# Optimization experiments

Measured on AMD Instinct MI355X. Metric: run time of the kernel, lower is better.

Reference implementation:

```python
import jax, jax.numpy as jnp
import numpy as np

D = 768      # d_model (BERT-base)
H = 8        # MatTransformer heads
DK = D // H  # 96
L = 4        # MatTransformer layers
FF = 1024    # MatTransformer hidden_size
NREL = 97    # num_relations
BAG = 8      # bag_len (docs per bag)
SEQ = 512    # seq_len
NB = 3       # bridge entities per doc
S = 2 + NB   # spans per doc: h, t, bridges
E = BAG * S  # total entities = 40
NEG = -1e30


def setup_inputs() -> dict:
    key = jax.random.key(0)
    ks = jax.random.split(key, 30)
    w = lambda k, shp: jax.random.normal(k, shp, jnp.float32) * 0.02
    inp = {
        "embedding": jax.random.normal(ks[0], (BAG, SEQ, D), jnp.float32),
        "spans": jnp.sort(jax.random.randint(ks[1], (BAG, S, 2), 0, SEQ, jnp.int32), axis=-1),
        # Codred pairwise-relation params (torch Linear stored as [in, out])
        "wu_w": w(ks[2], (D, D)), "wu_b": jnp.zeros((D,), jnp.float32),
        "wvv_w": w(ks[3], (D, D)), "wvv_b": jnp.zeros((D,), jnp.float32),
        "lnr_w": w(ks[4], (D, D)), "lnr_b": jnp.zeros((D,), jnp.float32),
        # MatTransformer params, stacked over layers
        "matt_wq": w(ks[5], (L, D, D)), "matt_bq": jnp.zeros((L, D), jnp.float32),
        "matt_wk": w(ks[6], (L, D, D)), "matt_bk": jnp.zeros((L, D), jnp.float32),
        "matt_wv": w(ks[7], (L, D, D)), "matt_bv": jnp.zeros((L, D), jnp.float32),
        "matt_wo": w(ks[8], (L, D, D)), "matt_bo": jnp.zeros((L, D), jnp.float32),
        "matt_w1": w(ks[9], (L, D, FF)), "matt_b1": jnp.zeros((L, FF), jnp.float32),
        "matt_w2": w(ks[10], (L, FF, D)), "matt_b2": jnp.zeros((L, D), jnp.float32),
        "matt_g1": jnp.ones((L, D), jnp.float32), "matt_be1": jnp.zeros((L, D), jnp.float32),
        "matt_g2": jnp.ones((L, D), jnp.float32), "matt_be2": jnp.zeros((L, D), jnp.float32),
        # relation predictor
        "pred_w": w(ks[11], (D, NREL)), "pred_b": jnp.zeros((NREL,), jnp.float32),
    }
    return inp


def _layernorm(x, g, b, eps=1e-5):
    m = jnp.mean(x, axis=-1, keepdims=True)
    v = jnp.var(x, axis=-1, keepdims=True)
    return (x - m) * jax.lax.rsqrt(v + eps) * g + b


def reference(embedding, spans, wu_w, wu_b, wvv_w, wvv_b, lnr_w, lnr_b,
              matt_wq, matt_bq, matt_wk, matt_bk, matt_wv, matt_bv, matt_wo, matt_bo,
              matt_w1, matt_b1, matt_w2, matt_b2, matt_g1, matt_be1, matt_g2, matt_be2,
              pred_w, pred_b):
    # --- entity span max-pool (gather + max over inclusive [start, end]) ---
    pos = jnp.arange(SEQ)
    span_mask = (pos[None, None, :] >= spans[..., 0:1]) & (pos[None, None, :] <= spans[..., 1:2])  # [BAG,S,SEQ]
    pooled = jnp.max(jnp.where(span_mask[..., None], embedding[:, None, :, :], NEG), axis=2)  # [BAG,S,D]
    htb = pooled.reshape(E, D)  # per-doc order: h, t, b1..bNB (matches htb_embs stacking)

    # --- pairwise relation matrix: relu(ln1(relu(u_i + v_j))) ---
    u = htb @ wu_w + wu_b                       # [E,D]
    v = htb @ wvv_w + wvv_b                     # [E,D]
    alpha = jax.nn.relu(u[:, None, :] + v[None, :, :])          # [E,E,D]
    rel = jax.nn.relu(alpha @ lnr_w + lnr_b)                    # [E,E,D]

    # --- MatTransformer: encoder over the E*E relation tokens (rel_mask all ones) ---
    T = E * E
    x = rel.reshape(T, D)
    scale = 1.0 / np.sqrt(DK).astype(np.float32)
    for l in range(L):
        q = (x @ matt_wq[l] + matt_bq[l]).reshape(T, H, DK)
        k = (x @ matt_wk[l] + matt_bk[l]).reshape(T, H, DK)
        vv = (x @ matt_wv[l] + matt_bv[l]).reshape(T, H, DK)
        scores = jnp.einsum('thd,shd->hts', q, k) * scale       # [H,T,T]
        attn = jax.nn.softmax(scores, axis=-1)
        o = jnp.einsum('hts,shd->thd', attn, vv).reshape(T, D)
        o = o @ matt_wo[l] + matt_bo[l]
        x = _layernorm(x + o, matt_g1[l], matt_be1[l])
        ff = jax.nn.relu(x @ matt_w1[l] + matt_b1[l]) @ matt_w2[l] + matt_b2[l]
        x = _layernorm(x + ff, matt_g2[l], matt_be2[l])
    rel_m = x.reshape(E, E, D)

    # --- gather (h, t) relation features, predict, bag max-pool over logits ---
    h_pos = jnp.arange(BAG) * S      # head entity index per doc
    t_pos = h_pos + 1                # tail entity index per doc
    ht_feat = rel_m[h_pos, t_pos]    # [BAG,D]
    ht_logits = ht_feat @ pred_w + pred_b          # [BAG,NREL]
    bag_logit = jnp.max(ht_logits, axis=0, keepdims=True)  # [1,NREL]
    return bag_logit
```

## Files before the change

kernel.cpp:

```cpp
#include <hip/hip_runtime.h>


#define D    768
#define H    8
#define DKD  96
#define LAY  4
#define FFD  1024
#define NREL 97
#define BAG  8
#define SPANS 5
#define E    40
#define TT   1600
#define SEQ  512
#define D3   2304
#define NS   3

typedef __attribute__((ext_vector_type(8))) short bf16x8;
typedef __attribute__((ext_vector_type(4))) float f32x4;
typedef unsigned short ushort_t;
typedef unsigned int uint_t;

__device__ __forceinline__ ushort_t f2b(float x) {
    uint_t u = __builtin_bit_cast(uint_t, x);
    return (ushort_t)((u + 0x7fffu + ((u >> 16) & 1u)) >> 16);
}
__device__ __forceinline__ float b2f(ushort_t v) {
    return __builtin_bit_cast(float, (uint_t)v << 16);
}

__device__ __forceinline__ void gload16(const void* g, void* l) {
    __builtin_amdgcn_global_load_lds(
        (const __attribute__((address_space(1))) unsigned int*)g,
        (__attribute__((address_space(3))) unsigned int*)l, 16, 0, 0);
}

__device__ __forceinline__ float block_sum(float v, float* red) {
#pragma unroll
    for (int o = 32; o >= 1; o >>= 1) v += __shfl_xor(v, o);
    __syncthreads();
    if ((threadIdx.x & 63) == 0) red[threadIdx.x >> 6] = v;
    __syncthreads();
    return red[0] + red[1] + red[2] + red[3];
}

__global__ __launch_bounds__(256) void span_pool_p1(const float* __restrict__ emb,
        const int* __restrict__ spans, float* __restrict__ partial) {
    const int e = blockIdx.x, pg = blockIdx.y;
    const int bag = e / SPANS;
    const int st = spans[e * 2 + 0];
    const int en = spans[e * 2 + 1];
    const int p0 = max(st, pg * 64);
    const int p1 = min(en, pg * 64 + 63);
    const int tid = threadIdx.x;
    if (tid >= 192) return;
    float4 m = make_float4(-1e30f, -1e30f, -1e30f, -1e30f);
    for (int p = p0; p <= p1; ++p) {
        const float4 v = *(const float4*)(emb + ((size_t)bag * SEQ + p) * D + tid * 4);
        m.x = fmaxf(m.x, v.x); m.y = fmaxf(m.y, v.y);
        m.z = fmaxf(m.z, v.z); m.w = fmaxf(m.w, v.w);
    }
    *(float4*)(partial + ((size_t)e * 8 + pg) * D + tid * 4) = m;
}

__global__ __launch_bounds__(256) void span_pool_p2(const float* __restrict__ partial,
        ushort_t* __restrict__ htb) {
    const int e = blockIdx.x;
    const int tid = threadIdx.x;
    if (tid >= 192) return;
    float4 m = make_float4(-1e30f, -1e30f, -1e30f, -1e30f);
#pragma unroll
    for (int pg = 0; pg < 8; ++pg) {
        const float4 v = *(const float4*)(partial + ((size_t)e * 8 + pg) * D + tid * 4);
        m.x = fmaxf(m.x, v.x); m.y = fmaxf(m.y, v.y);
        m.z = fmaxf(m.z, v.z); m.w = fmaxf(m.w, v.w);
    }
    ushort4 o;
    o.x = f2b(m.x); o.y = f2b(m.y); o.z = f2b(m.z); o.w = f2b(m.w);
    *(ushort4*)(htb + (size_t)e * D + tid * 4) = o;
}

__global__ __launch_bounds__(256) void alpha_k(const float* __restrict__ uv,
        ushort_t* __restrict__ a) {
    const int ij = blockIdx.x;
    const int i = ij / E, j = ij % E;
    const int tid = threadIdx.x;
#pragma unroll
    for (int t2 = 0; t2 < 3; ++t2) {
        const int d = tid + t2 * 256;
        a[(size_t)ij * D + d] =
            f2b(fmaxf(uv[(size_t)i * 1536 + d] + uv[(size_t)j * 1536 + 768 + d], 0.f));
    }
}

__global__ __launch_bounds__(256) void transpose_up(const float* __restrict__ lnr,
        const float* __restrict__ wu, const float* __restrict__ wvv,
        ushort_t* __restrict__ lnrT, ushort_t* __restrict__ wuvT) {
    __shared__ float t[32][33];
    const int z = blockIdx.z;
    const float* src = (z == 0) ? lnr : (z == 1) ? wu : wvv;
    ushort_t* dst = (z == 0) ? lnrT : wuvT + (size_t)(z - 1) * D * D;
    const int n0 = blockIdx.x * 32, k0 = blockIdx.y * 32;
    const int tx = threadIdx.x & 31, ty = threadIdx.x >> 5;
#pragma unroll
    for (int i = 0; i < 4; ++i)
        t[ty + i * 8][tx] = src[(size_t)(k0 + ty + i * 8) * D + n0 + tx];
    __syncthreads();
#pragma unroll
    for (int i = 0; i < 4; ++i)
        dst[(size_t)(n0 + ty + i * 8) * D + k0 + tx] = f2b(t[tx][ty + i * 8]);
}

__global__ __launch_bounds__(256) void transpose_layer(const float* __restrict__ wq,
        const float* __restrict__ wk, const float* __restrict__ wv,
        const float* __restrict__ wo, const float* __restrict__ w1,
        const float* __restrict__ w2, int l, ushort_t* __restrict__ wT4,
        ushort_t* __restrict__ w1T, ushort_t* __restrict__ w2T) {
    __shared__ float t[32][33];
    const int z = blockIdx.z;
    const float* src; ushort_t* dst; int K, N;
    if (z < 4) {
        K = D; N = D;
        src = (z == 0 ? wq : z == 1 ? wk : z == 2 ? wv : wo) + (size_t)l * D * D;
        dst = wT4 + (size_t)z * D * D;
    } else if (z == 4) {
        K = D; N = FFD; src = w1 + (size_t)l * D * FFD; dst = w1T;
    } else {
        K = FFD; N = D; src = w2 + (size_t)l * FFD * D; dst = w2T;
    }
    const int n0 = blockIdx.x * 32, k0 = blockIdx.y * 32;
    if (n0 >= N || k0 >= K) return;
    const int tx = threadIdx.x & 31, ty = threadIdx.x >> 5;
#pragma unroll
    for (int i = 0; i < 4; ++i)
        t[ty + i * 8][tx] = src[(size_t)(k0 + ty + i * 8) * N + n0 + tx];
    __syncthreads();
#pragma unroll
    for (int i = 0; i < 4; ++i)
        dst[(size_t)(n0 + ty + i * 8) * K + k0 + tx] = f2b(t[tx][ty + i * 8]);
}

__global__ __launch_bounds__(256) void concat_bias(const float* __restrict__ bq,
        const float* __restrict__ bk, const float* __restrict__ bv,
        const float* __restrict__ bu, const float* __restrict__ bvv,
        float* __restrict__ bqkv, float* __restrict__ buv) {
    const int i = blockIdx.x * 256 + threadIdx.x;
    if (i < LAY * D3) {
        const int l = i / D3, j = i % D3;
        bqkv[i] = j < D ? bq[l * D + j] : j < 2 * D ? bk[l * D + j - D] : bv[l * D + j - 2 * D];
    }
    const int k = i - LAY * D3;
    if (k >= 0 && k < 2 * D) buv[k] = k < D ? bu[k] : bvv[k - D];
}

template<int RELU, int SCALEQ>
__global__ __launch_bounds__(256) void gemm_mfma(const ushort_t* __restrict__ A,
        const ushort_t* __restrict__ Bt, const float* __restrict__ bias,
        float* __restrict__ Cf, ushort_t* __restrict__ Cb, int M, int N, int K) {
    __shared__ ushort_t As[128 * 32];
    __shared__ ushort_t Bs[64 * 32];
    const int tid = threadIdx.x;
    const int lane = tid & 63, w = tid >> 6;
    const int l15 = lane & 15, lg = lane >> 4;
    const int bm = blockIdx.y * 128, bn = blockIdx.x * 64;
    const int wm = (w >> 1) * 64, wn = (w & 1) * 32;
    const int trA0 = w * 32 + (lane >> 2);
    const int trA1 = trA0 + 16;
    const int trB  = w * 16 + (lane >> 2);
    const int sc   = (lane & 3) * 8;
    const size_t rowA0 = (size_t)min(bm + trA0, M - 1) * K;
    const size_t rowA1 = (size_t)min(bm + trA1, M - 1) * K;
    const size_t rowB  = (size_t)(bn + trB) * K;
    ushort_t* asd0 = As + w * 1024;
    ushort_t* asd1 = As + w * 1024 + 512;
    ushort_t* bsd  = Bs + w * 512;

    f32x4 acc[4][2];
#pragma unroll
    for (int mi = 0; mi < 4; ++mi)
#pragma unroll
        for (int ni = 0; ni < 2; ++ni)
            acc[mi][ni] = (f32x4){0.f, 0.f, 0.f, 0.f};

    for (int k0 = 0; k0 < K; k0 += 32) {
        __syncthreads();
        gload16(A + rowA0 + k0 + sc, asd0);
        gload16(A + rowA1 + k0 + sc, asd1);
        gload16(Bt + rowB + k0 + sc, bsd);
        __syncthreads();
        bf16x8 af[4], bfr[2];
#pragma unroll
        for (int mi = 0; mi < 4; ++mi)
            af[mi] = *(const bf16x8*)&As[(wm + mi * 16 + l15) * 32 + lg * 8];
#pragma unroll
        for (int ni = 0; ni < 2; ++ni)
            bfr[ni] = *(const bf16x8*)&Bs[(wn + ni * 16 + l15) * 32 + lg * 8];
        __builtin_amdgcn_s_setprio(1);
#pragma unroll
        for (int mi = 0; mi < 4; ++mi)
#pragma unroll
            for (int ni = 0; ni < 2; ++ni)
                acc[mi][ni] = __builtin_amdgcn_mfma_f32_16x16x32_bf16(
                    af[mi], bfr[ni], acc[mi][ni], 0, 0, 0);
        __builtin_amdgcn_s_setprio(0);
    }
#pragma unroll
    for (int mi = 0; mi < 4; ++mi)
#pragma unroll
        for (int ni = 0; ni < 2; ++ni)
#pragma unroll
            for (int r = 0; r < 4; ++r) {
                const int row = bm + wm + mi * 16 + lg * 4 + r;
                if (row >= M) continue;
                const int col = bn + wn + ni * 16 + l15;
                float v = acc[mi][ni][r] + bias[col];
                if (RELU) v = fmaxf(v, 0.f);
                if (SCALEQ) { if (col < D) v *= 0.10206207261596577f; }
                if (Cf) Cf[(size_t)row * N + col] = v;
                if (Cb) Cb[(size_t)row * N + col] = f2b(v);
            }
}

__global__ __launch_bounds__(256) void attn_part(const ushort_t* __restrict__ qkv,
        ushort_t* __restrict__ Opart, float* __restrict__ ml) {
    __shared__ ushort_t Ks[64][104];
    __shared__ ushort_t Vt[96][76];
    __shared__ ushort_t Ps[4][16][72];
    const int q0 = blockIdx.x * 64;
    const int h = blockIdx.y;
    const int cch = blockIdx.z;
    const int t_lo = (cch * (TT / 64)) / NS;
    const int t_hi = ((cch + 1) * (TT / 64)) / NS;
    const int tid = threadIdx.x;
    const int lane = tid & 63, w = tid >> 6;
    const int l15 = lane & 15, lg = lane >> 4;

    int r_[3], c_[3];
#pragma unroll
    for (int i = 0; i < 3; ++i) {
        const int ch = i * 256 + tid;
        r_[i] = ch / 12; c_[i] = (ch % 12) * 8;
    }
    bf16x8 qfrag[3];
#pragma unroll
    for (int ks = 0; ks < 3; ++ks)
        qfrag[ks] = *(const bf16x8*)(qkv + (size_t)(q0 + w * 16 + l15) * D3
                                     + h * DKD + ks * 32 + lg * 8);
    uint4 kreg[3], vreg[3];
    {
        const int s0 = t_lo * 64;
#pragma unroll
        for (int i = 0; i < 3; ++i) {
            kreg[i] = *(const uint4*)(qkv + (size_t)(s0 + r_[i]) * D3 + D + h * DKD + c_[i]);
            vreg[i] = *(const uint4*)(qkv + (size_t)(s0 + r_[i]) * D3 + 2 * D + h * DKD + c_[i]);
        }
    }
    float m_run[4], l_run[4];
    f32x4 acc_o[6];
#pragma unroll
    for (int r = 0; r < 4; ++r) { m_run[r] = -1e30f; l_run[r] = 0.f; }
#pragma unroll
    for (int nt = 0; nt < 6; ++nt) acc_o[nt] = (f32x4){0.f, 0.f, 0.f, 0.f};

    for (int t = t_lo; t < t_hi; ++t) {
        __syncthreads();
#pragma unroll
        for (int i = 0; i < 3; ++i) {
            *(uint4*)&Ks[r_[i]][c_[i]] = kreg[i];
            const ushort_t* pv = (const ushort_t*)&vreg[i];
#pragma unroll
            for (int j = 0; j < 8; ++j) Vt[c_[i] + j][r_[i]] = pv[j];
        }
        __syncthreads();
        if (t + 1 < t_hi) {
            const int s0 = (t + 1) * 64;
#pragma unroll
            for (int i = 0; i < 3; ++i) {
                kreg[i] = *(const uint4*)(qkv + (size_t)(s0 + r_[i]) * D3 + D + h * DKD + c_[i]);
                vreg[i] = *(const uint4*)(qkv + (size_t)(s0 + r_[i]) * D3 + 2 * D + h * DKD + c_[i]);
            }
        }
        f32x4 accs[4];
#pragma unroll
        for (int ni = 0; ni < 4; ++ni) accs[ni] = (f32x4){0.f, 0.f, 0.f, 0.f};
        __builtin_amdgcn_s_setprio(1);
#pragma unroll
        for (int ks = 0; ks < 3; ++ks) {
#pragma unroll
            for (int ni = 0; ni < 4; ++ni) {
                const bf16x8 bk = *(const bf16x8*)&Ks[ni * 16 + l15][ks * 32 + lg * 8];
                accs[ni] = __builtin_amdgcn_mfma_f32_16x16x32_bf16(qfrag[ks], bk, accs[ni], 0, 0, 0);
            }
        }
        __builtin_amdgcn_s_setprio(0);
        float mx[4];
#pragma unroll
        for (int r = 0; r < 4; ++r) {
            mx[r] = fmaxf(fmaxf(accs[0][r], accs[1][r]), fmaxf(accs[2][r], accs[3][r]));
#pragma unroll
            for (int o = 1; o <= 8; o <<= 1) mx[r] = fmaxf(mx[r], __shfl_xor(mx[r], o));
        }
        const bool grow = (mx[0] > m_run[0] + 8.f) || (mx[1] > m_run[1] + 8.f) ||
                          (mx[2] > m_run[2] + 8.f) || (mx[3] > m_run[3] + 8.f);
        if (__any(grow)) {
#pragma unroll
            for (int r = 0; r < 4; ++r) {
                const float mnew = fmaxf(m_run[r], mx[r]);
                const float sf = __expf(m_run[r] - mnew);
                m_run[r] = mnew;
                l_run[r] *= sf;
#pragma unroll
                for (int nt = 0; nt < 6; ++nt) acc_o[nt][r] *= sf;
            }
        }
        float ps[4][4];
#pragma unroll
        for (int r = 0; r < 4; ++r) {
            float rs = 0.f;
#pragma unroll
            for (int ni = 0; ni < 4; ++ni) {
                ps[ni][r] = __expf(accs[ni][r] - m_run[r]);
                rs += ps[ni][r];
            }
#pragma unroll
            for (int o = 1; o <= 8; o <<= 1) rs += __shfl_xor(rs, o);
            l_run[r] += rs;
        }
#pragma unroll
        for (int ni = 0; ni < 4; ++ni)
#pragma unroll
            for (int r = 0; r < 4; ++r)
                Ps[w][lg * 4 + r][ni * 16 + l15] = f2b(ps[ni][r]);
        __builtin_amdgcn_s_setprio(1);
#pragma unroll
        for (int ks = 0; ks < 2; ++ks) {
            const bf16x8 ap = *(const bf16x8*)&Ps[w][l15][ks * 32 + lg * 8];
#pragma unroll
            for (int nt = 0; nt < 6; ++nt) {
                const bf16x8 bv = *(const bf16x8*)&Vt[nt * 16 + l15][ks * 32 + lg * 8];
                acc_o[nt] = __builtin_amdgcn_mfma_f32_16x16x32_bf16(ap, bv, acc_o[nt], 0, 0, 0);
            }
        }
        __builtin_amdgcn_s_setprio(0);
    }
    __syncthreads();
    ushort_t* scr = &Ks[0][0] + w * (16 * 104);
#pragma unroll
    for (int nt = 0; nt < 6; ++nt)
#pragma unroll
        for (int r = 0; r < 4; ++r)
            scr[(lg * 4 + r) * 104 + nt * 16 + l15] = f2b(acc_o[nt][r]);
    const size_t obase = (((size_t)cch * H + h) * TT + q0 + w * 16) * DKD;
#pragma unroll
    for (int ch = 0; ch < 3; ++ch) {
        const int idx = ch * 64 + lane;
        const int row = idx / 12;
        const int c16 = (idx % 12) * 8;
        const uint4 v = *(const uint4*)&scr[row * 104 + c16];
        *(uint4*)(Opart + obase + (size_t)row * DKD + c16) = v;
    }
    if (l15 == 0) {
#pragma unroll
        for (int r = 0; r < 4; ++r) {
            const int row = q0 + w * 16 + lg * 4 + r;
            float2* mlp = (float2*)ml;
            mlp[((size_t)cch * H + h) * TT + row] = make_float2(m_run[r], l_run[r]);
        }
    }
}

__global__ __launch_bounds__(256) void attn_combine(const ushort_t* __restrict__ Opart,
        const float* __restrict__ ml, ushort_t* __restrict__ O) {
    const int row = blockIdx.x;
    const int tid = threadIdx.x;
    const float2* mlp = (const float2*)ml;
#pragma unroll
    for (int kk = 0; kk < 3; ++kk) {
        const int col = tid + kk * 256;
        const int h = col / DKD, d = col % DKD;
        float m[NS], l[NS], M = -1e30f;
#pragma unroll
        for (int c = 0; c < NS; ++c) {
            const float2 v = mlp[((size_t)c * H + h) * TT + row];
            m[c] = v.x; l[c] = v.y; M = fmaxf(M, m[c]);
        }
        float L = 0.f, o = 0.f;
#pragma unroll
        for (int c = 0; c < NS; ++c) {
            const float e = __expf(m[c] - M);
            L += l[c] * e;
            o += b2f(Opart[(((size_t)c * H + h) * TT + row) * DKD + d]) * e;
        }
        O[(size_t)row * D + col] = f2b(o / L);
    }
}

__global__ __launch_bounds__(256) void add_ln(float* __restrict__ x,
        const float* __restrict__ y, const float* __restrict__ g,
        const float* __restrict__ b, ushort_t* __restrict__ xb) {
    __shared__ float red[4];
    const int row = blockIdx.x;
    const int tid = threadIdx.x;
    float vals[3];
    float s = 0.f;
#pragma unroll
    for (int i = 0; i < 3; ++i) {
        const int c = tid + i * 256;
        const float t = x[(size_t)row * D + c] + y[(size_t)row * D + c];
        vals[i] = t; s += t;
    }
    const float mean = block_sum(s, red) * (1.f / 768.f);
    float s2 = 0.f;
#pragma unroll
    for (int i = 0; i < 3; ++i) { const float dd = vals[i] - mean; s2 += dd * dd; }
    const float var = block_sum(s2, red) * (1.f / 768.f);
    const float inv = rsqrtf(var + 1e-5f);
#pragma unroll
    for (int i = 0; i < 3; ++i) {
        const int c = tid + i * 256;
        const float o = (vals[i] - mean) * inv * g[c] + b[c];
        x[(size_t)row * D + c] = o;
        xb[(size_t)row * D + c] = f2b(o);
    }
}

__global__ __launch_bounds__(256) void predict_k(const float* __restrict__ x,
        const float* __restrict__ pw, const float* __restrict__ pb,
        float* __restrict__ out) {
    __shared__ float red[4];
    const int r = blockIdx.x;
    const int tid = threadIdx.x;
    float best = -1e30f;
    for (int bag = 0; bag < BAG; ++bag) {
        const int row = (bag * SPANS) * E + (bag * SPANS + 1);
        const float* f = x + (size_t)row * D;
        float acc = 0.f;
        for (int d = tid; d < D; d += 256) acc += f[d] * pw[(size_t)d * NREL + r];
        best = fmaxf(best, block_sum(acc, red));
    }
    if (tid == 0) out[r] = best + pb[r];
}

extern "C" void kernel_launch(void* const* d_in, const int* in_sizes, int n_in,
                              void* d_out, int out_size, void* d_ws, size_t ws_size,
                              hipStream_t stream) {
    const float* emb  = (const float*)d_in[0];
    const int*  spans = (const int*)d_in[1];
    const float* wu_w = (const float*)d_in[2];  const float* wu_b = (const float*)d_in[3];
    const float* wvv_w= (const float*)d_in[4];  const float* wvv_b= (const float*)d_in[5];
    const float* lnr_w= (const float*)d_in[6];  const float* lnr_b= (const float*)d_in[7];
    const float* wq = (const float*)d_in[8];    const float* bq = (const float*)d_in[9];
    const float* wk = (const float*)d_in[10];   const float* bk = (const float*)d_in[11];
    const float* wv = (const float*)d_in[12];   const float* bv = (const float*)d_in[13];
    const float* wo = (const float*)d_in[14];   const float* bo = (const float*)d_in[15];
    const float* w1 = (const float*)d_in[16];   const float* b1 = (const float*)d_in[17];
    const float* w2 = (const float*)d_in[18];   const float* b2 = (const float*)d_in[19];
    const float* g1 = (const float*)d_in[20];   const float* be1= (const float*)d_in[21];
    const float* g2 = (const float*)d_in[22];   const float* be2= (const float*)d_in[23];
    const float* pw = (const float*)d_in[24];   const float* pb = (const float*)d_in[25];

    char* cur = (char*)d_ws;
    auto alloc = [&](size_t bytes) { char* p = cur; cur += (bytes + 255) & ~(size_t)255; return p; };
    ushort_t* htb  = (ushort_t*)alloc(E * D * 2);
    float*    uvb  = (float*)alloc((size_t)E * 1536 * 4);
    float*    part = (float*)alloc((size_t)E * 8 * D * 4);
    float*    x    = (float*)alloc((size_t)TT * D * 4);
    ushort_t* xb   = (ushort_t*)alloc((size_t)TT * D * 2);
    ushort_t* qkv  = (ushort_t*)alloc((size_t)TT * D3 * 2);
    ushort_t* ob   = (ushort_t*)alloc((size_t)TT * D * 2);
    float*    tb   = (float*)alloc((size_t)TT * D * 4);
    ushort_t* fb   = (ushort_t*)alloc((size_t)TT * FFD * 2);
    ushort_t* wT4  = (ushort_t*)alloc((size_t)4 * D * D * 2);
    ushort_t* w1T  = (ushort_t*)alloc((size_t)D * FFD * 2);
    ushort_t* w2T  = (ushort_t*)alloc((size_t)FFD * D * 2);
    float*    bqkv = (float*)alloc((size_t)LAY * D3 * 4);
    float*    buv  = (float*)alloc((size_t)2 * D * 4);
    ushort_t* Opart = (ushort_t*)tb;
    float*    ml    = part;
    ushort_t* wuvT  = wT4;
    ushort_t* lnrT  = w1T;

    const int DD = D * D;

    span_pool_p1<<<dim3(E, 8), 256, 0, stream>>>(emb, spans, part);
    span_pool_p2<<<E, 256, 0, stream>>>(part, htb);
    transpose_up<<<dim3(24, 24, 3), 256, 0, stream>>>(lnr_w, wu_w, wvv_w, lnrT, wuvT);
    concat_bias<<<(LAY * D3 + 2 * D + 255) / 256, 256, 0, stream>>>(bq, bk, bv, wu_b, wvv_b, bqkv, buv);
    gemm_mfma<0, 0><<<dim3(1536 / 64, 1), 256, 0, stream>>>(htb, wuvT, buv, uvb, nullptr, E, 1536, D);
    alpha_k<<<TT, 256, 0, stream>>>(uvb, ob);
    gemm_mfma<1, 0><<<dim3(D / 64, (TT + 127) / 128), 256, 0, stream>>>(ob, lnrT, lnr_b, x, xb, TT, D, D);

    for (int l = 0; l < LAY; ++l) {
        transpose_layer<<<dim3(32, 32, 6), 256, 0, stream>>>(wq, wk, wv, wo, w1, w2, l, wT4, w1T, w2T);
        gemm_mfma<0, 1><<<dim3(D3 / 64, (TT + 127) / 128), 256, 0, stream>>>(
            xb, wT4, bqkv + l * D3, nullptr, qkv, TT, D3, D);
        attn_part<<<dim3(TT / 64, H, NS), 256, 0, stream>>>(qkv, Opart, ml);
        attn_combine<<<TT, 256, 0, stream>>>(Opart, ml, ob);
        gemm_mfma<0, 0><<<dim3(D / 64, (TT + 127) / 128), 256, 0, stream>>>(
            ob, wT4 + 3 * DD, bo + l * D, tb, nullptr, TT, D, D);
        add_ln<<<TT, 256, 0, stream>>>(x, tb, g1 + l * D, be1 + l * D, xb);
        gemm_mfma<1, 0><<<dim3(FFD / 64, (TT + 127) / 128), 256, 0, stream>>>(
            xb, w1T, b1 + l * FFD, nullptr, fb, TT, FFD, D);
        gemm_mfma<0, 0><<<dim3(D / 64, (TT + 127) / 128), 256, 0, stream>>>(
            fb, w2T, b2 + l * D, tb, nullptr, TT, D, FFD);
        add_ln<<<TT, 256, 0, stream>>>(x, tb, g2 + l * D, be2 + l * D, xb);
    }

    predict_k<<<NREL, 256, 0, stream>>>(x, pw, pb, (float*)d_out);
    (void)in_sizes; (void)n_in; (void)out_size; (void)ws_size;
}
```

Baseline: 673.5 us.

## Double-buffer GEMM LDS tiles and XOR-swizzle attention V transpose buffer

The GEMM kernel now uses two LDS buffers for A and B tiles, issuing loads for the next k-slice before computing on the current one, with one barrier per iteration instead of two. The attention kernel's transposed V buffer drops its padding and uses an XOR swizzle on the key column, applied on both write and read, to avoid LDS bank conflicts. The GEMM change doubles LDS use per block, which may reduce occupancy. The swizzle adds index arithmetic to every V read and write.

```diff
diff --git a/kernel.cpp b/kernel.cpp
--- a/kernel.cpp
+++ b/kernel.cpp
@@ -156,8 +156,8 @@
 __global__ __launch_bounds__(256) void gemm_mfma(const ushort_t* __restrict__ A,
         const ushort_t* __restrict__ Bt, const float* __restrict__ bias,
         float* __restrict__ Cf, ushort_t* __restrict__ Cb, int M, int N, int K) {
-    __shared__ ushort_t As[128 * 32];
-    __shared__ ushort_t Bs[64 * 32];
+    __shared__ ushort_t As[2][128 * 32];
+    __shared__ ushort_t Bs[2][64 * 32];
     const int tid = threadIdx.x;
     const int lane = tid & 63, w = tid >> 6;
     const int l15 = lane & 15, lg = lane >> 4;
@@ -170,9 +170,6 @@
     const size_t rowA0 = (size_t)min(bm + trA0, M - 1) * K;
     const size_t rowA1 = (size_t)min(bm + trA1, M - 1) * K;
     const size_t rowB  = (size_t)(bn + trB) * K;
-    ushort_t* asd0 = As + w * 1024;
-    ushort_t* asd1 = As + w * 1024 + 512;
-    ushort_t* bsd  = Bs + w * 512;
 
     f32x4 acc[4][2];
 #pragma unroll
@@ -181,19 +178,25 @@
         for (int ni = 0; ni < 2; ++ni)
             acc[mi][ni] = (f32x4){0.f, 0.f, 0.f, 0.f};
 
-    for (int k0 = 0; k0 < K; k0 += 32) {
-        __syncthreads();
-        gload16(A + rowA0 + k0 + sc, asd0);
-        gload16(A + rowA1 + k0 + sc, asd1);
-        gload16(Bt + rowB + k0 + sc, bsd);
-        __syncthreads();
+    auto STAGE = [&](int buf, int k0) {
+        gload16(A + rowA0 + k0 + sc, As[buf] + w * 1024);
+        gload16(A + rowA1 + k0 + sc, As[buf] + w * 1024 + 512);
+        gload16(Bt + rowB + k0 + sc, Bs[buf] + w * 512);
+    };
+
+    const int ntk = K / 32;
+    STAGE(0, 0);
+    __syncthreads();
+    for (int t = 0; t < ntk; ++t) {
+        const int buf = t & 1;
+        if (t + 1 < ntk) STAGE(buf ^ 1, (t + 1) * 32);
         bf16x8 af[4], bfr[2];
 #pragma unroll
         for (int mi = 0; mi < 4; ++mi)
-            af[mi] = *(const bf16x8*)&As[(wm + mi * 16 + l15) * 32 + lg * 8];
+            af[mi] = *(const bf16x8*)&As[buf][(wm + mi * 16 + l15) * 32 + lg * 8];
 #pragma unroll
         for (int ni = 0; ni < 2; ++ni)
-            bfr[ni] = *(const bf16x8*)&Bs[(wn + ni * 16 + l15) * 32 + lg * 8];
+            bfr[ni] = *(const bf16x8*)&Bs[buf][(wn + ni * 16 + l15) * 32 + lg * 8];
         __builtin_amdgcn_s_setprio(1);
 #pragma unroll
         for (int mi = 0; mi < 4; ++mi)
@@ -202,6 +205,7 @@
                 acc[mi][ni] = __builtin_amdgcn_mfma_f32_16x16x32_bf16(
                     af[mi], bfr[ni], acc[mi][ni], 0, 0, 0);
         __builtin_amdgcn_s_setprio(0);
+        __syncthreads();
     }
 #pragma unroll
     for (int mi = 0; mi < 4; ++mi)
@@ -223,7 +227,7 @@
 __global__ __launch_bounds__(256) void attn_part(const ushort_t* __restrict__ qkv,
         ushort_t* __restrict__ Opart, float* __restrict__ ml) {
     __shared__ ushort_t Ks[64][104];
-    __shared__ ushort_t Vt[96][76];
+    __shared__ ushort_t Vt[96][72];
     __shared__ ushort_t Ps[4][16][72];
     const int q0 = blockIdx.x * 64;
     const int h = blockIdx.y;
@@ -267,8 +271,9 @@
         for (int i = 0; i < 3; ++i) {
             *(uint4*)&Ks[r_[i]][c_[i]] = kreg[i];
             const ushort_t* pv = (const ushort_t*)&vreg[i];
-#pragma unroll
-            for (int j = 0; j < 8; ++j) Vt[c_[i] + j][r_[i]] = pv[j];
+            const int kk = r_[i] ^ (((c_[i] >> 3) & 7) << 3);
+#pragma unroll
+            for (int j = 0; j < 8; ++j) Vt[c_[i] + j][kk] = pv[j];
         }
         __syncthreads();
         if (t + 1 < t_hi) {
@@ -336,7 +341,9 @@
             const bf16x8 ap = *(const bf16x8*)&Ps[w][l15][ks * 32 + lg * 8];
 #pragma unroll
             for (int nt = 0; nt < 6; ++nt) {
-                const bf16x8 bv = *(const bf16x8*)&Vt[nt * 16 + l15][ks * 32 + lg * 8];
+                const int dim = nt * 16 + l15;
+                const int kcol = (ks * 32 + lg * 8) ^ (((dim >> 3) & 7) << 3);
+                const bf16x8 bv = *(const bf16x8*)&Vt[dim][kcol];
                 acc_o[nt] = __builtin_amdgcn_mfma_f32_16x16x32_bf16(ap, bv, acc_o[nt], 0, 0, 0);
             }
         }
```

Measured after the change: 629.7 us. 1.07x faster.
